# Performance work log

Measured on AMD Instinct MI355X. Metric: run time of the kernel, lower is better.

The kernel has to match this reference:

```python
import jax, jax.numpy as jnp
import numpy as np

WINDOW = 11
SIGMA = 1.5
CHANNELS = 3
C1 = 0.01 ** 2
C2 = 0.03 ** 2


def _gaussian_kernel(size=WINDOW, sigma=SIGMA, channels=CHANNELS):
    coords = jnp.arange(size, dtype=jnp.float32) - size // 2
    g = jnp.exp(-coords ** 2 / (2.0 * sigma ** 2))
    g = jnp.outer(g, g)
    g = g / g.sum()
    # depthwise kernel: [C, 1, K, K] (OIHW with feature_group_count=C)
    return jnp.broadcast_to(g[None, None], (channels, 1, size, size))


def _dwconv(x, kernel):
    # x: [N, C, H, W]; SAME padding, depthwise (groups = C)
    pad = WINDOW // 2
    return jax.lax.conv_general_dilated(
        x, kernel,
        window_strides=(1, 1),
        padding=[(pad, pad), (pad, pad)],
        dimension_numbers=('NCHW', 'OIHW', 'NCHW'),
        feature_group_count=CHANNELS,
    )


def setup_inputs() -> dict:
    key = jax.random.key(0)
    k1, k2 = jax.random.split(key)
    shape = (16, 3, 512, 512)
    pred = jax.random.uniform(k1, shape, dtype=jnp.float32)
    target = jax.random.uniform(k2, shape, dtype=jnp.float32)
    return {"pred": pred, "target": target}


def reference(pred, target):
    kernel = _gaussian_kernel().astype(pred.dtype)
    mu_p = _dwconv(pred, kernel)
    mu_t = _dwconv(target, kernel)
    mu_p2 = mu_p * mu_p
    mu_t2 = mu_t * mu_t
    mu_pt = mu_p * mu_t
    sigma_p2 = _dwconv(pred * pred, kernel) - mu_p2
    sigma_t2 = _dwconv(target * target, kernel) - mu_t2
    sigma_pt = _dwconv(pred * target, kernel) - mu_pt
    ssim_map = ((2.0 * mu_pt + C1) * (2.0 * sigma_pt + C2)) / (
        (mu_p2 + mu_t2 + C1) * (sigma_p2 + sigma_t2 + C2)
    )
    return 1.0 - ssim_map.mean()
```

## Files before the change

### kernel.cpp

```cpp
#include <hip/hip_runtime.h>
#include <math.h>

#define IMG_H 512
#define IMG_W 512
#define NSLOT 64
#define HT_S  56

typedef _Float16 f16x4 __attribute__((ext_vector_type(4)));
typedef _Float16 f16x8 __attribute__((ext_vector_type(8)));
typedef float    f32x4 __attribute__((ext_vector_type(4)));

__device__ const _Float16 WPAD[52] = {
    (_Float16)0.f,(_Float16)0.f,(_Float16)0.f,(_Float16)0.f,(_Float16)0.f,(_Float16)0.f,
    (_Float16)0.f,(_Float16)0.f,(_Float16)0.f,(_Float16)0.f,(_Float16)0.f,(_Float16)0.f,
    (_Float16)0.f,(_Float16)0.f,(_Float16)0.f,(_Float16)0.f,(_Float16)0.f,(_Float16)0.f,
    (_Float16)0.00102838f, (_Float16)0.00759876f, (_Float16)0.03600077f,
    (_Float16)0.10936065f, (_Float16)0.21300554f, (_Float16)0.26601173f,
    (_Float16)0.21300554f, (_Float16)0.10936065f, (_Float16)0.03600077f,
    (_Float16)0.00759876f, (_Float16)0.00102838f,
    (_Float16)0.f,(_Float16)0.f,(_Float16)0.f,(_Float16)0.f,(_Float16)0.f,(_Float16)0.f,
    (_Float16)0.f,(_Float16)0.f,(_Float16)0.f,(_Float16)0.f,(_Float16)0.f,(_Float16)0.f,
    (_Float16)0.f,(_Float16)0.f,(_Float16)0.f,(_Float16)0.f,(_Float16)0.f,(_Float16)0.f,
    (_Float16)0.f,(_Float16)0.f,(_Float16)0.f,(_Float16)0.f,(_Float16)0.f
};

__device__ __forceinline__ f16x8 frag_from_tab(int base)
{
    f16x8 f;
    #pragma unroll
    for (int j = 0; j < 8; ++j) f[j] = WPAD[base + j];
    return f;
}

__global__ __launch_bounds__(256, 6)
void ssim_main(const float* __restrict__ pred, const float* __restrict__ targ,
               float* __restrict__ partial, double* __restrict__ acc, int mode)
{
    __shared__ _Float16 hT[4][32][HT_S];

    const int tid  = threadIdx.x;
    const int lane = tid & 63, wave = tid >> 6;
    const int ln   = lane & 15, lg = lane >> 4;

    const int bid   = ((blockIdx.z << 4) + blockIdx.y) * 16 + blockIdx.x;
    const int chunk = (int)gridDim.z << 5;
    const int nb    = (bid & 7) * chunk + (bid >> 3);
    const int img   = nb >> 8;
    const int rem   = nb & 255;
    const int ty    = rem >> 4, tx = rem & 15;

    const float* __restrict__ p = pred + (size_t)img * (IMG_H * IMG_W);
    const float* __restrict__ t = targ + (size_t)img * (IMG_H * IMG_W);
    const int gr0 = ty * 32 - 5;
    const int wo  = tx * 32 - 8;

    const f16x8 Bw = frag_from_tab(15 + lg * 8 - ln);
    const f32x4 z = {0.f, 0.f, 0.f, 0.f};

    const int rtA = wave >> 1, ctA = wave & 1;
    const int grA = gr0 + rtA * 16 + ln;
    const int gcA = wo + ctA * 16 + lg * 8;
    const bool inA = ((unsigned)grA < (unsigned)IMG_H) &&
                     !(tx == 0 && ctA == 0 && lg == 0) &&
                     !(tx == 15 && ctA == 1 && lg == 3);
    const int grAc = grA < 0 ? 0 : (grA > IMG_H - 1 ? IMG_H - 1 : grA);
    const int gcAc = gcA < 0 ? 0 : (gcA > IMG_W - 8 ? IMG_W - 8 : gcA);
    const float* bpA = p + (size_t)grAc * IMG_W + gcAc;
    const float* btA = t + (size_t)grAc * IMG_W + gcAc;
    float4 pA0 = ((const float4*)bpA)[0], pA1 = ((const float4*)bpA)[1];
    float4 tA0 = ((const float4*)btA)[0], tA1 = ((const float4*)btA)[1];

    float4 pB0{}, pB1{}, tB0{}, tB1{};
    bool inB = false;
    if (wave < 2) {
        const int ctB = wave;
        const int grB = gr0 + 32 + ln;
        const int gcB = wo + ctB * 16 + lg * 8;
        inB = ((unsigned)grB < (unsigned)IMG_H) &&
              !(tx == 0 && ctB == 0 && lg == 0) &&
              !(tx == 15 && ctB == 1 && lg == 3);
        const int grBc = grB < 0 ? 0 : (grB > IMG_H - 1 ? IMG_H - 1 : grB);
        const int gcBc = gcB < 0 ? 0 : (gcB > IMG_W - 8 ? IMG_W - 8 : gcB);
        const float* bpB = p + (size_t)grBc * IMG_W + gcBc;
        const float* btB = t + (size_t)grBc * IMG_W + gcBc;
        pB0 = ((const float4*)bpB)[0]; pB1 = ((const float4*)bpB)[1];
        tB0 = ((const float4*)btB)[0]; tB1 = ((const float4*)btB)[1];
    }

    const f16x8 A2w = frag_from_tab(18 + lg * 8 - ln);

    auto conv_tile = [&](const float4& a0, const float4& a1,
                         const float4& b0, const float4& b1,
                         bool in, int ocol, int orow) {
        const _Float16 mh = in ? (_Float16)1.0f : (_Float16)0.0f;
        const f16x8 mv = {mh, mh, mh, mh, mh, mh, mh, mh};
        f16x8 s8 = f16x8{
            (_Float16)(a0.x + b0.x), (_Float16)(a0.y + b0.y),
            (_Float16)(a0.z + b0.z), (_Float16)(a0.w + b0.w),
            (_Float16)(a1.x + b1.x), (_Float16)(a1.y + b1.y),
            (_Float16)(a1.z + b1.z), (_Float16)(a1.w + b1.w)} * mv;
        f16x8 d8 = f16x8{
            (_Float16)(a0.x - b0.x), (_Float16)(a0.y - b0.y),
            (_Float16)(a0.z - b0.z), (_Float16)(a0.w - b0.w),
            (_Float16)(a1.x - b1.x), (_Float16)(a1.y - b1.y),
            (_Float16)(a1.z - b1.z), (_Float16)(a1.w - b1.w)} * mv;
        f16x8 fq[4];
        fq[0] = s8; fq[1] = d8;
        fq[2] = s8 * s8; fq[3] = d8 * d8;
        #pragma unroll
        for (int q = 0; q < 4; ++q) {
            f32x4 dd = __builtin_amdgcn_mfma_f32_16x16x32_f16(fq[q], Bw, z, 0, 0, 0);
            *(f16x4*)&hT[q][ocol][orow] =
                f16x4{(_Float16)dd[0], (_Float16)dd[1], (_Float16)dd[2], (_Float16)dd[3]};
        }
    };
    conv_tile(pA0, pA1, tA0, tA1, inA, ctA * 16 + ln, rtA * 16 + lg * 4);
    if (wave < 2)
        conv_tile(pB0, pB1, tB0, tB1, inB, wave * 16 + ln, 32 + lg * 4);
    __syncthreads();

    float lsum = 0.f;
    {
        const int ctv = wave & 1, rtv = wave >> 1;
        const int ocol  = ctv * 16 + ln;
        const int rbase = rtv * 16 + lg * 8;
        f32x4 accq[4];
        #pragma unroll
        for (int q = 0; q < 4; ++q) {
            f16x8 b = *(const f16x8*)&hT[q][ocol][rbase];
            accq[q] = __builtin_amdgcn_mfma_f32_16x16x32_f16(A2w, b, z, 0, 0, 0);
        }
        const float C1 = 1e-4f, C2 = 9e-4f;
        #pragma unroll
        for (int r = 0; r < 4; ++r) {
            float F1 = accq[0][r], F2 = accq[1][r];
            float F3 = accq[2][r], F4 = accq[3][r];
            float a = F1 * F1, b = F2 * F2;
            float mpmt2 = 0.5f * (a - b);
            float msq   = 0.5f * (a + b);
            float cpt2  = 0.5f * (F3 - F4) - mpmt2;
            float vsum  = 0.5f * (F3 + F4) - msq;
            float num = (mpmt2 + C1) * (cpt2 + C2);
            float den = (msq + C1) * (vsum + C2);
            lsum = fmaf(num, __builtin_amdgcn_rcpf(den), lsum);
        }
    }

    #pragma unroll
    for (int off = 32; off > 0; off >>= 1)
        lsum += __shfl_down(lsum, off, 64);
    if (lane == 0) {
        if (mode == 0) partial[nb * 4 + wave] = lsum;
        else atomicAdd(&acc[(nb * 4 + wave) & (NSLOT - 1)], (double)lsum);
    }
}

__global__ void ssim_init(double* acc)
{
    if (threadIdx.x < NSLOT) acc[threadIdx.x] = 0.0;
}

__global__ __launch_bounds__(1024)
void ssim_fin_slots(const float* __restrict__ partial, float* __restrict__ out,
                    int n4, double inv_n)
{
    __shared__ double red[16];
    double s = 0.0;
    const int tid = threadIdx.x;
    for (int i = tid; i < n4; i += 1024) {
        float4 v = ((const float4*)partial)[i];
        s += (double)v.x + (double)v.y + (double)v.z + (double)v.w;
    }
    #pragma unroll
    for (int off = 32; off > 0; off >>= 1)
        s += __shfl_down(s, off, 64);
    if ((tid & 63) == 0) red[tid >> 6] = s;
    __syncthreads();
    if (tid == 0) {
        double tot = 0.0;
        #pragma unroll
        for (int w = 0; w < 16; ++w) tot += red[w];
        out[0] = (float)(1.0 - tot * inv_n);
    }
}

__global__ void ssim_fin_atomic(const double* __restrict__ acc, float* __restrict__ out,
                                double inv_n)
{
    if (threadIdx.x == 0) {
        double s = 0.0;
        for (int i = 0; i < NSLOT; ++i) s += acc[i];
        out[0] = (float)(1.0 - s * inv_n);
    }
}

extern "C" void kernel_launch(void* const* d_in, const int* in_sizes, int n_in,
                              void* d_out, int out_size, void* d_ws, size_t ws_size,
                              hipStream_t stream)
{
    const float* pred = (const float*)d_in[0];
    const float* targ = (const float*)d_in[1];
    float* out = (float*)d_out;

    const long long total = (long long)in_sizes[0];
    const int n_img = (int)(total / (IMG_H * IMG_W));
    dim3 grid(IMG_W / 32, IMG_H / 32, n_img);
    const int nblk = grid.x * grid.y * grid.z;
    const int nslots = nblk * 4;
    const double inv_n = 1.0 / (double)total;

    if (ws_size >= (size_t)nslots * sizeof(float)) {
        float* partial = (float*)d_ws;
        hipLaunchKernelGGL(ssim_main, grid, dim3(256), 0, stream,
                           pred, targ, partial, (double*)nullptr, 0);
        hipLaunchKernelGGL(ssim_fin_slots, dim3(1), dim3(1024), 0, stream,
                           partial, out, nslots / 4, inv_n);
    } else {
        double* acc = (double*)d_ws;
        hipLaunchKernelGGL(ssim_init, dim3(1), dim3(64), 0, stream, acc);
        hipLaunchKernelGGL(ssim_main, grid, dim3(256), 0, stream,
                           pred, targ, (float*)nullptr, acc, 1);
        hipLaunchKernelGGL(ssim_fin_atomic, dim3(1), dim3(1), 0, stream,
                           acc, out, inv_n);
    }
}
```

Measured before the change: 150.4 us.

## Give each wave its own 16x32 strip and private swizzled LDS buffer

Each block now covers a 64x32 output tile (half as many blocks), and each wave owns a 16-column strip. The wave loads three 16-row input tiles for its strip, runs the horizontal MFMA pass into its own XOR-swizzled LDS region, and then runs two vertical MFMA passes. Because the LDS buffer is private to the wave, the block-wide __syncthreads is replaced by an lgkmcnt wait, and global loads are interleaved with compute to hide latency. The cost is more MFMA work per wave, fewer blocks, and a halo-to-interior load ratio that is unchanged.

```diff
diff --git a/kernel.cpp b/kernel.cpp
--- a/kernel.cpp
+++ b/kernel.cpp
@@ -4,7 +4,6 @@
 #define IMG_H 512
 #define IMG_W 512
 #define NSLOT 64
-#define HT_S  56
 
 typedef _Float16 f16x4 __attribute__((ext_vector_type(4)));
 typedef _Float16 f16x8 __attribute__((ext_vector_type(8)));
@@ -32,66 +31,54 @@
     return f;
 }
 
+#define HT_BYTES (4 * 4 * 16 * 48 * 2)
+
 __global__ __launch_bounds__(256, 6)
 void ssim_main(const float* __restrict__ pred, const float* __restrict__ targ,
                float* __restrict__ partial, double* __restrict__ acc, int mode)
 {
-    __shared__ _Float16 hT[4][32][HT_S];
+    __shared__ __align__(128) _Float16 hT[4][4][16][48];
 
     const int tid  = threadIdx.x;
     const int lane = tid & 63, wave = tid >> 6;
     const int ln   = lane & 15, lg = lane >> 4;
 
-    const int bid   = ((blockIdx.z << 4) + blockIdx.y) * 16 + blockIdx.x;
-    const int chunk = (int)gridDim.z << 5;
+    const int bid   = ((blockIdx.z * 16 + blockIdx.y) * 8) + blockIdx.x;
+    const int chunk = (int)gridDim.z << 4;
     const int nb    = (bid & 7) * chunk + (bid >> 3);
-    const int img   = nb >> 8;
-    const int rem   = nb & 255;
-    const int ty    = rem >> 4, tx = rem & 15;
+    const int img   = nb >> 7;
+    const int rem   = nb & 127;
+    const int ty    = rem >> 3, tx = rem & 7;
 
     const float* __restrict__ p = pred + (size_t)img * (IMG_H * IMG_W);
     const float* __restrict__ t = targ + (size_t)img * (IMG_H * IMG_W);
+
     const int gr0 = ty * 32 - 5;
-    const int wo  = tx * 32 - 8;
-
-    const f16x8 Bw = frag_from_tab(15 + lg * 8 - ln);
+    const int wo  = tx * 64 + wave * 16 - 8;
+
+    const f16x8 Bw  = frag_from_tab(15 + lg * 8 - ln);
+    const f16x8 A2w = frag_from_tab(18 + lg * 8 - ln);
     const f32x4 z = {0.f, 0.f, 0.f, 0.f};
 
-    const int rtA = wave >> 1, ctA = wave & 1;
-    const int grA = gr0 + rtA * 16 + ln;
-    const int gcA = wo + ctA * 16 + lg * 8;
-    const bool inA = ((unsigned)grA < (unsigned)IMG_H) &&
-                     !(tx == 0 && ctA == 0 && lg == 0) &&
-                     !(tx == 15 && ctA == 1 && lg == 3);
-    const int grAc = grA < 0 ? 0 : (grA > IMG_H - 1 ? IMG_H - 1 : grA);
-    const int gcAc = gcA < 0 ? 0 : (gcA > IMG_W - 8 ? IMG_W - 8 : gcA);
-    const float* bpA = p + (size_t)grAc * IMG_W + gcAc;
-    const float* btA = t + (size_t)grAc * IMG_W + gcAc;
-    float4 pA0 = ((const float4*)bpA)[0], pA1 = ((const float4*)bpA)[1];
-    float4 tA0 = ((const float4*)btA)[0], tA1 = ((const float4*)btA)[1];
-
-    float4 pB0{}, pB1{}, tB0{}, tB1{};
-    bool inB = false;
-    if (wave < 2) {
-        const int ctB = wave;
-        const int grB = gr0 + 32 + ln;
-        const int gcB = wo + ctB * 16 + lg * 8;
-        inB = ((unsigned)grB < (unsigned)IMG_H) &&
-              !(tx == 0 && ctB == 0 && lg == 0) &&
-              !(tx == 15 && ctB == 1 && lg == 3);
-        const int grBc = grB < 0 ? 0 : (grB > IMG_H - 1 ? IMG_H - 1 : grB);
-        const int gcBc = gcB < 0 ? 0 : (gcB > IMG_W - 8 ? IMG_W - 8 : gcB);
-        const float* bpB = p + (size_t)grBc * IMG_W + gcBc;
-        const float* btB = t + (size_t)grBc * IMG_W + gcBc;
-        pB0 = ((const float4*)bpB)[0]; pB1 = ((const float4*)bpB)[1];
-        tB0 = ((const float4*)btB)[0]; tB1 = ((const float4*)btB)[1];
-    }
-
-    const f16x8 A2w = frag_from_tab(18 + lg * 8 - ln);
-
-    auto conv_tile = [&](const float4& a0, const float4& a1,
-                         const float4& b0, const float4& b1,
-                         bool in, int ocol, int orow) {
+    const int  gc    = wo + lg * 8;
+    const bool colOK = (gc >= 0) && (gc <= IMG_W - 8);
+    const int  gcc   = gc < 0 ? 0 : (gc > IMG_W - 8 ? IMG_W - 8 : gc);
+
+    int  grr[3]; bool ok[3];
+    const float *bp[3], *bt[3];
+    #pragma unroll
+    for (int rt = 0; rt < 3; ++rt) {
+        const int gr = gr0 + rt * 16 + ln;
+        ok[rt] = ((unsigned)gr < (unsigned)IMG_H) && colOK;
+        const int grc = gr < 0 ? 0 : (gr > IMG_H - 1 ? IMG_H - 1 : gr);
+        grr[rt] = grc;
+        bp[rt] = p + (size_t)grc * IMG_W + gcc;
+        bt[rt] = t + (size_t)grc * IMG_W + gcc;
+    }
+
+    const int swz = (ln & 4) << 2;
+
+    auto proc = [&](int rt, float4 a0, float4 a1, float4 b0, float4 b1, bool in) {
         const _Float16 mh = in ? (_Float16)1.0f : (_Float16)0.0f;
         const f16x8 mv = {mh, mh, mh, mh, mh, mh, mh, mh};
         f16x8 s8 = f16x8{
@@ -107,30 +94,39 @@
         f16x8 fq[4];
         fq[0] = s8; fq[1] = d8;
         fq[2] = s8 * s8; fq[3] = d8 * d8;
+        const int woff = ((rt * 16 + lg * 4) * 2) ^ swz;
         #pragma unroll
         for (int q = 0; q < 4; ++q) {
             f32x4 dd = __builtin_amdgcn_mfma_f32_16x16x32_f16(fq[q], Bw, z, 0, 0, 0);
-            *(f16x4*)&hT[q][ocol][orow] =
+            *(f16x4*)((char*)&hT[wave][q][ln][0] + woff) =
                 f16x4{(_Float16)dd[0], (_Float16)dd[1], (_Float16)dd[2], (_Float16)dd[3]};
         }
     };
-    conv_tile(pA0, pA1, tA0, tA1, inA, ctA * 16 + ln, rtA * 16 + lg * 4);
-    if (wave < 2)
-        conv_tile(pB0, pB1, tB0, tB1, inB, wave * 16 + ln, 32 + lg * 4);
-    __syncthreads();
+
+    float4 a00 = ((const float4*)bp[0])[0], a01 = ((const float4*)bp[0])[1];
+    float4 b00 = ((const float4*)bt[0])[0], b01 = ((const float4*)bt[0])[1];
+    float4 a10 = ((const float4*)bp[1])[0], a11 = ((const float4*)bp[1])[1];
+    float4 b10 = ((const float4*)bt[1])[0], b11 = ((const float4*)bt[1])[1];
+    proc(0, a00, a01, b00, b01, ok[0]);
+    float4 a20 = ((const float4*)bp[2])[0], a21 = ((const float4*)bp[2])[1];
+    float4 b20 = ((const float4*)bt[2])[0], b21 = ((const float4*)bt[2])[1];
+    proc(1, a10, a11, b10, b11, ok[1]);
+    proc(2, a20, a21, b20, b21, ok[2]);
+
+    asm volatile("s_waitcnt lgkmcnt(0)" ::: "memory");
+    __builtin_amdgcn_sched_barrier(0);
 
     float lsum = 0.f;
-    {
-        const int ctv = wave & 1, rtv = wave >> 1;
-        const int ocol  = ctv * 16 + ln;
-        const int rbase = rtv * 16 + lg * 8;
+    const float C1 = 1e-4f, C2 = 9e-4f;
+    #pragma unroll
+    for (int v = 0; v < 2; ++v) {
+        const int roff = ((v * 16 + lg * 8) * 2) ^ swz;
         f32x4 accq[4];
         #pragma unroll
         for (int q = 0; q < 4; ++q) {
-            f16x8 b = *(const f16x8*)&hT[q][ocol][rbase];
+            f16x8 b = *(const f16x8*)((char*)&hT[wave][q][ln][0] + roff);
             accq[q] = __builtin_amdgcn_mfma_f32_16x16x32_f16(A2w, b, z, 0, 0, 0);
         }
-        const float C1 = 1e-4f, C2 = 9e-4f;
         #pragma unroll
         for (int r = 0; r < 4; ++r) {
             float F1 = accq[0][r], F2 = accq[1][r];
@@ -204,7 +200,7 @@
 
     const long long total = (long long)in_sizes[0];
     const int n_img = (int)(total / (IMG_H * IMG_W));
-    dim3 grid(IMG_W / 32, IMG_H / 32, n_img);
+    dim3 grid(IMG_W / 64, IMG_H / 32, n_img);
     const int nblk = grid.x * grid.y * grid.z;
     const int nslots = nblk * 4;
     const double inv_n = 1.0 / (double)total;
```

After: 141.1 us. -6.2%, faster.
